# Kernel optimization log

Hardware: AMD Instinct MI355X
Metric: run time of the kernel (lower is better)

Reference implementation:

```python
import jax, jax.numpy as jnp
import numpy as np

EMBED = 768
HEADS = 12


def setup_inputs() -> dict:
    key = jax.random.key(0)
    k1, k2, k3 = jax.random.split(key, 3)
    B, N, E = 2, 2048, EMBED
    x = jax.random.normal(k1, (B, N, E), dtype=jnp.float32)
    w_qkv = jax.random.normal(k2, (3 * E, E), dtype=jnp.float32) * (1.0 / np.sqrt(E))
    b_qkv = jnp.zeros((3 * E,), dtype=jnp.float32)
    w_o = jax.random.normal(k3, (E, E), dtype=jnp.float32) * (1.0 / np.sqrt(E))
    b_o = jnp.zeros((E,), dtype=jnp.float32)
    return {"x": x, "w_qkv": w_qkv, "b_qkv": b_qkv, "w_o": w_o, "b_o": b_o}


def reference(x, w_qkv, b_qkv, w_o, b_o):
    B, N, E = x.shape
    H = HEADS
    d = E // H
    # fused qkv projection (torch Linear: x @ W^T + b)
    qkv = x @ w_qkv.T + b_qkv                       # [B, N, 3E]
    # Rearrange 'b n (h qkv e) -> b qkv h n e'
    qkv = qkv.reshape(B, N, H, 3, d).transpose(0, 3, 2, 1, 4)  # [B, 3, H, N, d]
    q, k, v = qkv[:, 0], qkv[:, 1], qkv[:, 2]       # each [B, H, N, d]
    scores = jnp.einsum("bhqd,bhkd->bhqk", q, k)    # [B, H, N, N]
    attn = jax.nn.softmax(scores / jnp.sqrt(jnp.float32(E)), axis=-1)
    ctx = jnp.einsum("bhqk,bhkd->bhqd", attn, v)    # [B, H, N, d]
    ctx = ctx.transpose(0, 2, 1, 3).reshape(B, N, E)  # 'b h n d -> b n (h d)'
    out = ctx @ w_o.T + b_o
    return out
```

## Files before the change

kernel.cpp:

```cpp
#include <hip/hip_runtime.h>

#define BB 2
#define NN 2048
#define EE 768
#define HH 12
#define DD 64
#define MM (BB*NN)
#define E3 (3*EE)
#define QSCALE 0.05205877280961602f

typedef __bf16 bf16x8 __attribute__((ext_vector_type(8)));
typedef float  f32x4  __attribute__((ext_vector_type(4)));
typedef unsigned short u16x8 __attribute__((ext_vector_type(8)));
typedef unsigned short u16x4 __attribute__((ext_vector_type(4)));
typedef short s16x4 __attribute__((ext_vector_type(4)));
typedef unsigned int u32x2 __attribute__((ext_vector_type(2)));

#define MFMA(a,b,c)   __builtin_amdgcn_mfma_f32_16x16x32_bf16(a,b,c,0,0,0)
#define MFMA16(a,b,c) __builtin_amdgcn_mfma_f32_16x16x16bf16_1k(a,b,c,0,0,0)

__device__ __forceinline__ unsigned short f2bf(float f) {
    unsigned int u = __float_as_uint(f);
    u += 0x7FFFu + ((u >> 16) & 1u);
    return (unsigned short)(u >> 16);
}

typedef __attribute__((address_space(3))) unsigned int as3u32;
typedef __attribute__((address_space(1))) unsigned int as1u32;
__device__ __forceinline__ void gll16(const void* g, void* l) {
    __builtin_amdgcn_global_load_lds((const as1u32*)(uintptr_t)g,
                                     (as3u32*)(unsigned int)(uintptr_t)l, 16, 0, 0);
}

#define XB4 786432
#define WQ4 442368
#define WO4 147456
__global__ __launch_bounds__(256)
void cast3(const float* __restrict__ x, const float* __restrict__ wq,
           const float* __restrict__ wo, unsigned short* __restrict__ dst) {
    int i = blockIdx.x * 256 + threadIdx.x;
    const float* src;
    int off;
    if (i < XB4)            { src = x;  off = i; }
    else if (i < XB4+WQ4)   { src = wq; off = i - XB4; }
    else                    { src = wo; off = i - XB4 - WQ4; }
    float4 v = ((const float4*)src)[off];
    ushort4 o;
    o.x = f2bf(v.x); o.y = f2bf(v.y); o.z = f2bf(v.z); o.w = f2bf(v.w);
    ((ushort4*)dst)[i] = o;
}

__global__ __launch_bounds__(256)
void gemm_qkv(const unsigned short* __restrict__ A, const unsigned short* __restrict__ W,
              const float* __restrict__ bias,
              unsigned short* __restrict__ o0, unsigned short* __restrict__ o1,
              unsigned short* __restrict__ o2)
{
    __shared__ unsigned short As[128 * 32];
    __shared__ unsigned short Bs[128 * 32];

    const int tid = threadIdx.x;
    const int l = tid & 63;
    const int w = tid >> 6;
    const int m0 = blockIdx.x * 128;
    const int c0 = blockIdx.y * 128;
    const int wm = (w >> 1) * 64;
    const int wn = (w & 1) * 64;

    const int s0 = w * 2;
    const unsigned short* a_src0 = A + (size_t)(m0 + s0*16      + (l>>2)) * EE + (l&3)*8;
    const unsigned short* a_src1 = A + (size_t)(m0 + (s0+1)*16  + (l>>2)) * EE + (l&3)*8;
    const unsigned short* b_src0 = W + (size_t)(c0 + s0*16      + (l>>2)) * EE + (l&3)*8;
    const unsigned short* b_src1 = W + (size_t)(c0 + (s0+1)*16  + (l>>2)) * EE + (l&3)*8;
    unsigned short* a_dst0 = &As[s0*512];
    unsigned short* a_dst1 = &As[(s0+1)*512];
    unsigned short* b_dst0 = &Bs[s0*512];
    unsigned short* b_dst1 = &Bs[(s0+1)*512];

    const f32x4 zero4 = {0.f, 0.f, 0.f, 0.f};
    f32x4 acc[4][4];
    #pragma unroll
    for (int i = 0; i < 4; ++i)
        #pragma unroll
        for (int j = 0; j < 4; ++j) acc[i][j] = zero4;

    for (int k0 = 0; k0 < EE; k0 += 32) {
        __syncthreads();
        gll16(a_src0 + k0, a_dst0);
        gll16(a_src1 + k0, a_dst1);
        gll16(b_src0 + k0, b_dst0);
        gll16(b_src1 + k0, b_dst1);
        __syncthreads();

        bf16x8 af[4], bf[4];
        #pragma unroll
        for (int i = 0; i < 4; ++i)
            af[i] = *(const bf16x8*)&As[(wm + 16*i + (l&15))*32 + (l>>4)*8];
        #pragma unroll
        for (int j = 0; j < 4; ++j)
            bf[j] = *(const bf16x8*)&Bs[(wn + 16*j + (l&15))*32 + (l>>4)*8];
        #pragma unroll
        for (int i = 0; i < 4; ++i)
            #pragma unroll
            for (int j = 0; j < 4; ++j)
                acc[i][j] = MFMA(af[i], bf[j], acc[i][j]);
    }

    const int sec = (c0 + wn) >> 6;
    const int hh = sec / 3;
    const int tt = sec - hh*3;
    #pragma unroll
    for (int j = 0; j < 4; ++j) {
        const int col = c0 + wn + 16*j + (l&15);
        const int dcol = 16*j + (l&15);
        const float bj = bias[col];
        #pragma unroll
        for (int i = 0; i < 4; ++i) {
            const int row0 = m0 + wm + 16*i + (l>>4)*4;
            const int b = row0 >> 11;
            const int n = row0 & (NN - 1);
            if (tt == 2) {
                ushort4 pk;
                pk.x = f2bf(acc[i][j][0] + bj);
                pk.y = f2bf(acc[i][j][1] + bj);
                pk.z = f2bf(acc[i][j][2] + bj);
                pk.w = f2bf(acc[i][j][3] + bj);
                *(ushort4*)&o2[(((size_t)b*HH + hh)*DD + dcol)*NN + n] = pk;
            } else {
                unsigned short* dst = (tt == 0) ? o0 : o1;
                #pragma unroll
                for (int r = 0; r < 4; ++r) {
                    float val = acc[i][j][r] + bj;
                    if (tt == 0) val *= QSCALE;
                    dst[(((size_t)b*HH + hh)*NN + n + r)*DD + dcol] = f2bf(val);
                }
            }
        }
    }
}

__global__ __launch_bounds__(256)
void gemm_out(const unsigned short* __restrict__ A, const unsigned short* __restrict__ W,
              const float* __restrict__ bias, float* __restrict__ of)
{
    __shared__ unsigned short As[64 * 32];
    __shared__ unsigned short Bs[128 * 32];

    const int tid = threadIdx.x;
    const int l = tid & 63;
    const int w = tid >> 6;
    const int m0 = blockIdx.x * 64;
    const int c0 = blockIdx.y * 128;
    const int wm = (w >> 1) * 32;
    const int wn = (w & 1) * 64;

    const unsigned short* s_src[3];
    unsigned short* s_dst[3];
    #pragma unroll
    for (int s = 0; s < 3; ++s) {
        const int ch = 3*w + s;
        if (ch < 4) {
            s_src[s] = A + (size_t)(m0 + ch*16 + (l>>2)) * EE + (l&3)*8;
            s_dst[s] = &As[ch*512];
        } else {
            s_src[s] = W + (size_t)(c0 + (ch-4)*16 + (l>>2)) * EE + (l&3)*8;
            s_dst[s] = &Bs[(ch-4)*512];
        }
    }

    const f32x4 zero4 = {0.f, 0.f, 0.f, 0.f};
    f32x4 acc[2][4];
    #pragma unroll
    for (int i = 0; i < 2; ++i)
        #pragma unroll
        for (int j = 0; j < 4; ++j) acc[i][j] = zero4;

    for (int k0 = 0; k0 < EE; k0 += 32) {
        __syncthreads();
        #pragma unroll
        for (int s = 0; s < 3; ++s) gll16(s_src[s] + k0, s_dst[s]);
        __syncthreads();

        bf16x8 af[2], bf[4];
        #pragma unroll
        for (int i = 0; i < 2; ++i)
            af[i] = *(const bf16x8*)&As[(wm + 16*i + (l&15))*32 + (l>>4)*8];
        #pragma unroll
        for (int j = 0; j < 4; ++j)
            bf[j] = *(const bf16x8*)&Bs[(wn + 16*j + (l&15))*32 + (l>>4)*8];
        #pragma unroll
        for (int i = 0; i < 2; ++i)
            #pragma unroll
            for (int j = 0; j < 4; ++j)
                acc[i][j] = MFMA(af[i], bf[j], acc[i][j]);
    }

    #pragma unroll
    for (int j = 0; j < 4; ++j) {
        const int col = c0 + wn + 16*j + (l&15);
        const float bj = bias[col];
        #pragma unroll
        for (int i = 0; i < 2; ++i) {
            #pragma unroll
            for (int r = 0; r < 4; ++r) {
                const int row = m0 + wm + 16*i + (l>>4)*4 + r;
                of[(size_t)row * EE + col] = acc[i][j][r] + bj;
            }
        }
    }
}

__global__ __launch_bounds__(256, 3)
void attn_mfma(const unsigned short* __restrict__ Qg, const unsigned short* __restrict__ K,
               const unsigned short* __restrict__ Vt_g, unsigned short* __restrict__ ctx)
{
    __shared__ unsigned char smem[35840];
    unsigned short* Qs = (unsigned short*)smem;
    float* Red = (float*)smem;
    float* Ls  = (float*)(smem + 34816);

    const int tid = threadIdx.x;
    const int l = tid & 63;
    const int w = tid >> 6;
    const int quad = l >> 4;
    const int lc = l & 15;

    const int id = blockIdx.x;
    const int bh = id % 24;
    const int bq = id / 24;
    const int b  = bh / 12;
    const int h  = bh - b*12;
    const size_t hb = (size_t)bh * NN * DD;

    const f32x4 zero4 = {0.f, 0.f, 0.f, 0.f};

    {
        const int row = tid >> 2;
        const int col = (tid & 3) * 16;
        const unsigned short* src = Qg + hb + (size_t)(bq*64 + row)*DD + col;
        u16x8 qa = *(const u16x8*)src;
        u16x8 qb2 = *(const u16x8*)(src + 8);
        *(u16x8*)&Qs[row*64 + col]     = qa;
        *(u16x8*)&Qs[row*64 + col + 8] = qb2;
    }
    __syncthreads();
    bf16x8 qf[4][2];
    #pragma unroll
    for (int g = 0; g < 4; ++g)
        #pragma unroll
        for (int ks = 0; ks < 2; ++ks)
            qf[g][ks] = *(const bf16x8*)&Qs[(g*16 + lc)*64 + ks*32 + quad*8];

    f32x4 O[4][4];
    #pragma unroll
    for (int db = 0; db < 4; ++db)
        #pragma unroll
        for (int g = 0; g < 4; ++g) O[db][g] = zero4;
    float lsum[4] = {0.f, 0.f, 0.f, 0.f};

    const unsigned short* kp = K + hb + (size_t)(w*16 + lc)*DD + quad*8;
    const unsigned short* vp[4];
    #pragma unroll
    for (int db = 0; db < 4; ++db)
        vp[db] = Vt_g + hb + (size_t)(db*16 + lc)*NN + w*16 + quad*4;

    u16x8 rk0 = *(const u16x8*)kp;
    u16x8 rk1 = *(const u16x8*)(kp + 32);
    kp += 64*DD;

    for (int t = 0; t < NN/64; ++t) {
        u16x4 rv[4];
        #pragma unroll
        for (int db = 0; db < 4; ++db) {
            rv[db] = *(const u16x4*)vp[db];
            vp[db] += 64;
        }

        bf16x8 kf0 = __builtin_bit_cast(bf16x8, rk0);
        bf16x8 kf1 = __builtin_bit_cast(bf16x8, rk1);
        f32x4 st[4];
        #pragma unroll
        for (int g = 0; g < 4; ++g) {
            f32x4 t0 = MFMA(kf0, qf[g][0], zero4);
            st[g] = MFMA(kf1, qf[g][1], t0);
        }

        rk0 = *(const u16x8*)kp;
        rk1 = *(const u16x8*)(kp + 32);
        kp += 64*DD;

        s16x4 pf[4];
        #pragma unroll
        for (int g = 0; g < 4; ++g) {
            float e0 = __builtin_amdgcn_exp2f(st[g][0]);
            float e1 = __builtin_amdgcn_exp2f(st[g][1]);
            float e2 = __builtin_amdgcn_exp2f(st[g][2]);
            float e3 = __builtin_amdgcn_exp2f(st[g][3]);
            lsum[g] += (e0 + e1) + (e2 + e3);
            unsigned int p01 = __builtin_amdgcn_perm(__float_as_uint(e1) + 0x8000u,
                                                     __float_as_uint(e0) + 0x8000u, 0x07060302u);
            unsigned int p23 = __builtin_amdgcn_perm(__float_as_uint(e3) + 0x8000u,
                                                     __float_as_uint(e2) + 0x8000u, 0x07060302u);
            u32x2 pp = {p01, p23};
            pf[g] = __builtin_bit_cast(s16x4, pp);
        }

        #pragma unroll
        for (int db = 0; db < 4; ++db) {
            s16x4 vfr = __builtin_bit_cast(s16x4, rv[db]);
            #pragma unroll
            for (int g = 0; g < 4; ++g)
                O[db][g] = MFMA16(vfr, pf[g], O[db][g]);
        }
    }

    #pragma unroll
    for (int g = 0; g < 4; ++g) {
        lsum[g] += __shfl_xor(lsum[g], 16);
        lsum[g] += __shfl_xor(lsum[g], 32);
    }
    __syncthreads();
    if (quad == 0) {
        #pragma unroll
        for (int g = 0; g < 4; ++g) Ls[w*64 + g*16 + lc] = lsum[g];
    }
    if (w & 1) {
        float* R = Red + (w >> 1) * 4352;
        #pragma unroll
        for (int db = 0; db < 4; ++db)
            #pragma unroll
            for (int g = 0; g < 4; ++g)
                *(f32x4*)&R[(g*16 + lc)*68 + db*16 + quad*4] = O[db][g];
    }
    __syncthreads();
    if (!(w & 1)) {
        float* R = Red + (w >> 1) * 4352;
        #pragma unroll
        for (int db = 0; db < 4; ++db)
            #pragma unroll
            for (int g = 0; g < 4; ++g)
                O[db][g] += *(const f32x4*)&R[(g*16 + lc)*68 + db*16 + quad*4];
    }
    __syncthreads();
    if (w == 2) {
        #pragma unroll
        for (int db = 0; db < 4; ++db)
            #pragma unroll
            for (int g = 0; g < 4; ++g)
                *(f32x4*)&Red[(g*16 + lc)*68 + db*16 + quad*4] = O[db][g];
    }
    __syncthreads();
    if (w == 0) {
        float inv[4];
        #pragma unroll
        for (int g = 0; g < 4; ++g) {
            const int q = g*16 + lc;
            inv[g] = 1.f / (Ls[q] + Ls[64 + q] + Ls[128 + q] + Ls[192 + q]);
        }
        #pragma unroll
        for (int db = 0; db < 4; ++db) {
            #pragma unroll
            for (int g = 0; g < 4; ++g) {
                f32x4 o = O[db][g] + *(const f32x4*)&Red[(g*16 + lc)*68 + db*16 + quad*4];
                ushort4 pk;
                pk.x = f2bf(o[0] * inv[g]);
                pk.y = f2bf(o[1] * inv[g]);
                pk.z = f2bf(o[2] * inv[g]);
                pk.w = f2bf(o[3] * inv[g]);
                const int n = bq*64 + g*16 + lc;
                *(ushort4*)&ctx[((size_t)(b*NN + n))*EE + h*DD + db*16 + quad*4] = pk;
            }
        }
    }
}

extern "C" void kernel_launch(void* const* d_in, const int* in_sizes, int n_in,
                              void* d_out, int out_size, void* d_ws, size_t ws_size,
                              hipStream_t stream)
{
    const float* x     = (const float*)d_in[0];
    const float* w_qkv = (const float*)d_in[1];
    const float* b_qkv = (const float*)d_in[2];
    const float* w_o   = (const float*)d_in[3];
    const float* b_o   = (const float*)d_in[4];
    float* out = (float*)d_out;

    unsigned short* wsu = (unsigned short*)d_ws;
    const size_t XB = (size_t)MM * EE;
    const size_t WQ = (size_t)E3 * EE;
    const size_t WO = (size_t)EE * EE;
    const size_t HS = (size_t)BB * HH * NN * DD;
    unsigned short* xb   = wsu;
    unsigned short* wqb  = xb  + XB;
    unsigned short* wob  = wqb + WQ;
    unsigned short* qb   = wob + WO;
    unsigned short* kb   = qb  + HS;
    unsigned short* vtb  = kb  + HS;
    unsigned short* ctxb = vtb + HS;

    cast3<<<(XB4 + WQ4 + WO4)/256, 256, 0, stream>>>(x, w_qkv, w_o, xb);

    dim3 g1(MM/128, E3/128);
    gemm_qkv<<<g1, 256, 0, stream>>>(xb, wqb, b_qkv, qb, kb, vtb);

    attn_mfma<<<768, 256, 0, stream>>>(qb, kb, vtb, ctxb);

    dim3 g3(MM/64, EE/128);
    gemm_out<<<g3, 256, 0, stream>>>(ctxb, wob, b_o, out);
}
```

Before: 199.6 us.

## Stage K and V tiles through swizzled shared memory in attention loop

The attention kernel now loads each 64-key K tile and V^T tile cooperatively with coalesced 16-element global loads into LDS, using an XOR swizzle for K and a padded stride for V. Each wave then reads its MFMA fragments from LDS instead of issuing strided per-wave global loads. The aim is better global coalescing. In exchange it adds two block barriers per tile and drops the register prefetch of the next K tile, so load latency is no longer overlapped. The launch-bounds occupancy hint of 3 is also removed.

Result: faster. 191.9 us (-3.8%).

```diff
diff --git a/kernel.cpp b/kernel.cpp
--- a/kernel.cpp
+++ b/kernel.cpp
@@ -12,7 +12,6 @@
 typedef __bf16 bf16x8 __attribute__((ext_vector_type(8)));
 typedef float  f32x4  __attribute__((ext_vector_type(4)));
 typedef unsigned short u16x8 __attribute__((ext_vector_type(8)));
-typedef unsigned short u16x4 __attribute__((ext_vector_type(4)));
 typedef short s16x4 __attribute__((ext_vector_type(4)));
 typedef unsigned int u32x2 __attribute__((ext_vector_type(2)));
 
@@ -210,12 +209,14 @@
     }
 }
 
-__global__ __launch_bounds__(256, 3)
+__global__ __launch_bounds__(256)
 void attn_mfma(const unsigned short* __restrict__ Qg, const unsigned short* __restrict__ K,
                const unsigned short* __restrict__ Vt_g, unsigned short* __restrict__ ctx)
 {
     __shared__ unsigned char smem[35840];
     unsigned short* Qs = (unsigned short*)smem;
+    unsigned short* Ks = (unsigned short*)smem;
+    unsigned short* Vt = (unsigned short*)(smem + 16384);
     float* Red = (float*)smem;
     float* Ls  = (float*)(smem + 34816);
 
@@ -224,6 +225,7 @@
     const int w = tid >> 6;
     const int quad = l >> 4;
     const int lc = l & 15;
+    const int x7 = lc & 7;
 
     const int id = blockIdx.x;
     const int bh = id % 24;
@@ -258,36 +260,40 @@
         for (int g = 0; g < 4; ++g) O[db][g] = zero4;
     float lsum[4] = {0.f, 0.f, 0.f, 0.f};
 
-    const unsigned short* kp = K + hb + (size_t)(w*16 + lc)*DD + quad*8;
-    const unsigned short* vp[4];
-    #pragma unroll
-    for (int db = 0; db < 4; ++db)
-        vp[db] = Vt_g + hb + (size_t)(db*16 + lc)*NN + w*16 + quad*4;
-
-    u16x8 rk0 = *(const u16x8*)kp;
-    u16x8 rk1 = *(const u16x8*)(kp + 32);
-    kp += 64*DD;
-
-    for (int t = 0; t < NN/64; ++t) {
-        u16x4 rv[4];
-        #pragma unroll
-        for (int db = 0; db < 4; ++db) {
-            rv[db] = *(const u16x4*)vp[db];
-            vp[db] += 64;
-        }
-
-        bf16x8 kf0 = __builtin_bit_cast(bf16x8, rk0);
-        bf16x8 kf1 = __builtin_bit_cast(bf16x8, rk1);
+    const int srow = tid >> 2;
+    const int sc = tid & 3;
+    const unsigned short* kbase = K + hb + (size_t)srow*DD + sc*16;
+    const unsigned short* vbase = Vt_g + hb + (size_t)srow*NN + sc*16;
+    const int c0s = ((2*sc)     ^ (srow & 7)) * 8;
+    const int c1s = ((2*sc + 1) ^ (srow & 7)) * 8;
+
+    const int krow = (16*w + lc) * 64;
+    const int chq0 = ((    quad) ^ x7) * 8;
+    const int chq1 = ((4 + quad) ^ x7) * 8;
+    const int voff = 16*w + quad*4;
+
+    for (int kt = 0; kt < NN/64; ++kt) {
+        const unsigned short* ksrc = kbase + (size_t)kt*64*DD;
+        const unsigned short* vsrc = vbase + kt*64;
+        u16x8 k0 = *(const u16x8*)ksrc;
+        u16x8 k1 = *(const u16x8*)(ksrc + 8);
+        u16x8 v0 = *(const u16x8*)vsrc;
+        u16x8 v1 = *(const u16x8*)(vsrc + 8);
+        __syncthreads();
+        *(u16x8*)&Ks[srow*64 + c0s] = k0;
+        *(u16x8*)&Ks[srow*64 + c1s] = k1;
+        *(u16x8*)&Vt[srow*72 + sc*16]     = v0;
+        *(u16x8*)&Vt[srow*72 + sc*16 + 8] = v1;
+        __syncthreads();
+
+        bf16x8 kf0 = *(const bf16x8*)&Ks[krow + chq0];
+        bf16x8 kf1 = *(const bf16x8*)&Ks[krow + chq1];
         f32x4 st[4];
         #pragma unroll
         for (int g = 0; g < 4; ++g) {
             f32x4 t0 = MFMA(kf0, qf[g][0], zero4);
             st[g] = MFMA(kf1, qf[g][1], t0);
         }
-
-        rk0 = *(const u16x8*)kp;
-        rk1 = *(const u16x8*)(kp + 32);
-        kp += 64*DD;
 
         s16x4 pf[4];
         #pragma unroll
@@ -307,7 +313,7 @@
 
         #pragma unroll
         for (int db = 0; db < 4; ++db) {
-            s16x4 vfr = __builtin_bit_cast(s16x4, rv[db]);
+            s16x4 vfr = *(const s16x4*)&Vt[(16*db + lc)*72 + voff];
             #pragma unroll
             for (int g = 0; g < 4; ++g)
                 O[db][g] = MFMA16(vfr, pf[g], O[db][g]);
```
